# Performance work log

Hardware: AMD Instinct MI355X
Metric: run time of the kernel (lower is better)

## Reference

```python
import jax, jax.numpy as jnp
import numpy as np

WINDOW_SIZE = 11
SIGMA = 1.5
DATA_RANGE = 1.0
CHANNEL = 3
K1 = 0.01
K2 = 0.03
EPS = 1e-08


def _gaussian_window(window_size, sigma, channel):
    # 1D gaussian normalized to sum 1, then outer product -> 2D window
    xs = np.arange(window_size) - window_size // 2
    g = np.exp(-(xs.astype(np.float32) ** 2) / (2.0 * sigma ** 2))
    g = g / g.sum()
    w2d = np.outer(g, g).astype(np.float32)  # [K, K]
    # depthwise kernel in OIHW layout: [channel, 1, K, K]
    return jnp.asarray(np.broadcast_to(w2d, (channel, 1, window_size, window_size)))


def _depthwise_blur(img, window):
    # img: [B, C, H, W], window: [C, 1, K, K]; SAME padding depthwise conv
    pad = WINDOW_SIZE // 2
    return jax.lax.conv_general_dilated(
        img, window,
        window_strides=(1, 1),
        padding=[(pad, pad), (pad, pad)],
        dimension_numbers=("NCHW", "OIHW", "NCHW"),
        feature_group_count=CHANNEL,
    )


def setup_inputs() -> dict:
    key = jax.random.key(0)
    kx, ky = jax.random.split(key)
    x = jax.random.uniform(kx, (32, 3, 512, 512), dtype=jnp.float32)
    y = jax.random.uniform(ky, (32, 3, 512, 512), dtype=jnp.float32)
    return {"x": x, "y": y}


def reference(x, y):
    window = _gaussian_window(WINDOW_SIZE, SIGMA, CHANNEL)
    C1 = (K1 * DATA_RANGE) ** 2
    C2 = (K2 * DATA_RANGE) ** 2

    mu_x = _depthwise_blur(x, window)
    mu_y = _depthwise_blur(y, window)
    mu_x2 = mu_x * mu_x
    mu_y2 = mu_y * mu_y
    mu_xy = mu_x * mu_y

    sigma_x2 = _depthwise_blur(x * x, window) - mu_x2
    sigma_y2 = _depthwise_blur(y * y, window) - mu_y2
    sigma_xy = _depthwise_blur(x * y, window) - mu_xy

    num = (2.0 * mu_xy + C1) * (2.0 * sigma_xy + C2)
    den = (mu_x2 + mu_y2 + C1) * (sigma_x2 + sigma_y2 + C2)
    ssim_map = num / (den + EPS)
    return 1.0 - jnp.mean(ssim_map)
```

## Files before the change

### kernel.cpp

```cpp
#include <hip/hip_runtime.h>

typedef float v4f   __attribute__((ext_vector_type(4)));
typedef float f32x4 __attribute__((ext_vector_type(4)));
typedef _Float16 h4 __attribute__((ext_vector_type(4)));
typedef _Float16 h8 __attribute__((ext_vector_type(8)));

#define HH 512
#define WW 512
#define NPLANES 96
#define NSTRIP 32
#define NUNIT (NPLANES * NSTRIP)
#define WPB 4
#define NBLK (NUNIT / WPB)
#define C1V 1e-4f
#define C2V 9e-4f
#define EPSV 1e-8f
#define NPIX 25165824.0f

#define SLOT_B 640
#define Q_B    1920
#define WAVE_B 9600
#define LDS_B  (WPB * WAVE_B)

#define MF(A, B) __builtin_amdgcn_mfma_f32_16x16x32_f16((A), (B), zf, 0, 0, 0)

#define SELW(DST, IX) { const int ix_ = (IX); float r_ = 0.f; \
  r_ = (ix_ == 0) ? wv0 : r_;  r_ = (ix_ == 1) ? wv1 : r_; \
  r_ = (ix_ == 2) ? wv2 : r_;  r_ = (ix_ == 3) ? wv3 : r_; \
  r_ = (ix_ == 4) ? wv4 : r_;  r_ = (ix_ == 5) ? wv5 : r_; \
  r_ = (ix_ == 6) ? wv6 : r_;  r_ = (ix_ == 7) ? wv7 : r_; \
  r_ = (ix_ == 8) ? wv8 : r_;  r_ = (ix_ == 9) ? wv9 : r_; \
  r_ = (ix_ == 10) ? wv10 : r_; DST = r_; }

#define PACK8(DST, F0,F1,F2,F3,F4,F5,F6,F7) \
  DST = (h8){(_Float16)(F0),(_Float16)(F1),(_Float16)(F2),(_Float16)(F3), \
             (_Float16)(F4),(_Float16)(F5),(_Float16)(F6),(_Float16)(F7)};

#define EPX(M) { \
  const float mux_ = mx[M], muy_ = my[M]; \
  const float mx2_ = mux_ * mux_, my2_ = muy_ * muy_, mxy_ = mux_ * muy_; \
  const float sx2_ = vx2[M] - mx2_, sy2_ = vy2[M] - my2_, sxy_ = vxy[M] - mxy_; \
  const float num_ = fmaf(2.f, mxy_, C1V) * fmaf(2.f, sxy_, C2V); \
  const float den_ = (mx2_ + my2_ + C1V) * (sx2_ + sy2_ + C2V) + EPSV; \
  acc##M = fmaf(num_, __builtin_amdgcn_rcpf(den_), acc##M); }

#define VLOADL(O) { \
  const int c_ = (O) - 1 + ((s + 1) >> 1); \
  const char* rb_ = wlds + ((c_ + 3) % 3) * SLOT_B + rByte; \
  vbx  = *(const h8*)(rb_); \
  vby  = *(const h8*)(rb_ + Q_B); \
  vbx2 = *(const h8*)(rb_ + 2 * Q_B); \
  vby2 = *(const h8*)(rb_ + 3 * Q_B); \
  vbxy = *(const h8*)(rb_ + 4 * Q_B); }

#define VMFMA { \
  const f32x4 mx  = MF(Wf, vbx);  const f32x4 my  = MF(Wf, vby); \
  const f32x4 vx2 = MF(Wf, vbx2); const f32x4 vy2 = MF(Wf, vby2); \
  const f32x4 vxy = MF(Wf, vbxy); \
  EPX(0) EPX(1) EPX(2) EPX(3) }

#define STEP(TT, CXA,CXB,CYA,CYB) { \
  const int tt_ = (TT); \
  if (tt_ >= 3) VLOADL(tt_ - 3) \
  h8 ax, ay; \
  PACK8(ax, CXA[0],CXA[1],CXA[2],CXA[3], CXB[0],CXB[1],CXB[2],CXB[3]) \
  PACK8(ay, CYA[0],CYA[1],CYA[2],CYA[3], CYB[0],CYB[1],CYB[2],CYB[3]) \
  if (tt_ < 32) { \
    const int rb2_ = min(max(16 * (tt_ + 1), 0), 496); \
    const float* qx_ = xp + (size_t)rb2_ * WW; \
    const float* qy_ = yp + (size_t)rb2_ * WW; \
    CXA = *(const v4f*)(qx_ + offA); CXB = *(const v4f*)(qx_ + offB); \
    CYA = *(const v4f*)(qy_ + offA); CYB = *(const v4f*)(qy_ + offB); \
  } \
  const bool rOK_ = (unsigned)(tt_ - 1) < 32u; \
  const h8 wfh_ = rOK_ ? WfH : (h8)(_Float16)0.f; \
  const h8 ax2 = ax * ax, ay2 = ay * ay, axy = ax * ay; \
  const f32x4 chx  = MF(ax,  wfh_); const f32x4 chy  = MF(ay,  wfh_); \
  const f32x4 chx2 = MF(ax2, wfh_); const f32x4 chy2 = MF(ay2, wfh_); \
  const f32x4 chxy = MF(axy, wfh_); \
  { char* wb_ = wlds + ((tt_ + 2) % 3) * SLOT_B + wByte; \
    *(h4*)(wb_)         = (h4){(_Float16)chx[0], (_Float16)chx[1], (_Float16)chx[2], (_Float16)chx[3]}; \
    *(h4*)(wb_ + Q_B)   = (h4){(_Float16)chy[0], (_Float16)chy[1], (_Float16)chy[2], (_Float16)chy[3]}; \
    *(h4*)(wb_ + 2*Q_B) = (h4){(_Float16)chx2[0],(_Float16)chx2[1],(_Float16)chx2[2],(_Float16)chx2[3]}; \
    *(h4*)(wb_ + 3*Q_B) = (h4){(_Float16)chy2[0],(_Float16)chy2[1],(_Float16)chy2[2],(_Float16)chy2[3]}; \
    *(h4*)(wb_ + 4*Q_B) = (h4){(_Float16)chxy[0],(_Float16)chxy[1],(_Float16)chxy[2],(_Float16)chxy[3]}; } \
  if (tt_ >= 3) VMFMA }

__global__ __launch_bounds__(64 * WPB)
void ssim_main(const float* __restrict__ x, const float* __restrict__ y,
               float* __restrict__ partial)
{
  __shared__ __attribute__((aligned(16))) char lds[LDS_B];

  const int l = threadIdx.x & 63;
  const int wid = threadIdx.x >> 6;
  const int n = l & 15;
  const int s = l >> 4;

  const int wg = blockIdx.x;
  const int swz = (wg & 7) * (NBLK / 8) + (wg >> 3);
  const int unit = swz * WPB + wid;
  const int plane = unit >> 5;
  const int strip = unit & 31;
  const int C0 = strip * 16;

  char* wlds = lds + wid * WAVE_B;

  const float* xp = x + (size_t)plane * (HH * WW);
  const float* yp = y + (size_t)plane * (HH * WW);

  float wv0, wv1, wv2, wv3, wv4, wv5, wv6, wv7, wv8, wv9, wv10;
#define WINIT(k) wv##k = expf(-((float)((k - 5) * (k - 5))) / 4.5f);
  WINIT(0) WINIT(1) WINIT(2) WINIT(3) WINIT(4) WINIT(5)
  WINIT(6) WINIT(7) WINIT(8) WINIT(9) WINIT(10)
#undef WINIT
  const float inv_ = 1.f / (wv0 + wv1 + wv2 + wv3 + wv4 + wv5 + wv6 + wv7 + wv8 + wv9 + wv10);
#define WNORM(k) wv##k = __int_as_float(__builtin_amdgcn_readfirstlane(__float_as_int(wv##k * inv_)));
  WNORM(0) WNORM(1) WNORM(2) WNORM(3) WNORM(4) WNORM(5)
  WNORM(6) WNORM(7) WNORM(8) WNORM(9) WNORM(10)
#undef WNORM

  const f32x4 zf = {0.f, 0.f, 0.f, 0.f};

  h8 Wf;
  {
    const int kb = 8 * s;
    float b0,b1,b2,b3,b4,b5,b6,b7;
    SELW(b0, kb + 0 - n - 3) SELW(b1, kb + 1 - n - 3)
    SELW(b2, kb + 2 - n - 3) SELW(b3, kb + 3 - n - 3)
    SELW(b4, kb + 4 - n - 3) SELW(b5, kb + 5 - n - 3)
    SELW(b6, kb + 6 - n - 3) SELW(b7, kb + 7 - n - 3)
    PACK8(Wf, b0,b1,b2,b3,b4,b5,b6,b7)
  }

  const int cb = C0 - 8 + 8 * s;
  const bool kill = (cb < 0) || (cb >= WW);
  h8 WfH = Wf;
  if (kill) WfH = (h8)(_Float16)0.f;
  const int ca = kill ? 0 : cb;

  const int offA = n * WW + ca;
  const int offB = offA + 4;

  const int wByte = n * 40 + 8 * s;
  const int rByte = n * 40 + 16 * ((s + 1) & 1);

  h8 vbx, vby, vbx2, vby2, vbxy;
  float acc0 = 0.f, acc1 = 0.f, acc2 = 0.f, acc3 = 0.f;

  v4f XA0, XB0, YA0, YB0, XA1, XB1, YA1, YB1;
  XA0 = *(const v4f*)(xp + offA); XB0 = *(const v4f*)(xp + offB);
  YA0 = *(const v4f*)(yp + offA); YB0 = *(const v4f*)(yp + offB);
  XA1 = XA0; XB1 = XB0; YA1 = YA0; YB1 = YB0;

  #pragma unroll 1
  for (int u = 0; u < 17; ++u) {
    STEP(2 * u,     XA0, XB0, YA0, YB0)
    STEP(2 * u + 1, XA1, XB1, YA1, YB1)
  }
  VLOADL(31) VMFMA

  float a = (acc0 + acc1) + (acc2 + acc3);
  #pragma unroll
  for (int off = 32; off > 0; off >>= 1) a += __shfl_down(a, off);
  if (l == 0) partial[unit] = a;
}

__global__ void finalize_kernel(const float* __restrict__ partial, float* __restrict__ out)
{
  __shared__ float s4[4];
  float a = 0.f;
  for (int i = threadIdx.x; i < NUNIT; i += 256) a += partial[i];
  #pragma unroll
  for (int off = 32; off > 0; off >>= 1) a += __shfl_down(a, off);
  if ((threadIdx.x & 63) == 0) s4[threadIdx.x >> 6] = a;
  __syncthreads();
  if (threadIdx.x == 0) out[0] = 1.f - (s4[0] + s4[1] + s4[2] + s4[3]) * (1.f / NPIX);
}

extern "C" void kernel_launch(void* const* d_in, const int* in_sizes, int n_in,
                              void* d_out, int out_size, void* d_ws, size_t ws_size,
                              hipStream_t stream)
{
  const float* x = (const float*)d_in[0];
  const float* y = (const float*)d_in[1];
  float* ws = (float*)d_ws;
  float* out = (float*)d_out;

  hipLaunchKernelGGL(ssim_main, dim3(NBLK), dim3(64 * WPB), 0, stream, x, y, ws);
  hipLaunchKernelGGL(finalize_kernel, dim3(1), dim3(256), 0, stream, ws, out);
}
```

Baseline: 74.76 us.

## Split each wave's column strip into two interleaved half-height chains

Each wave now processes its 512-row strip as two independent chains (top and bottom halves) interleaved step by step, each with its own LDS ring and accumulators. Workgroups shrink to two waves and the per-wave LDS doubles, with a waves-per-EU hint added. The goal is more instruction-level parallelism per wave, so MFMA, LDS and global-load latencies of one chain overlap with work from the other. In exchange it raises register pressure, adds halo rows at the chain boundary, and lowers the wave count per block.

```diff
diff --git a/kernel.cpp b/kernel.cpp
--- a/kernel.cpp
+++ b/kernel.cpp
@@ -10,7 +10,7 @@
 #define NPLANES 96
 #define NSTRIP 32
 #define NUNIT (NPLANES * NSTRIP)
-#define WPB 4
+#define WPB 2
 #define NBLK (NUNIT / WPB)
 #define C1V 1e-4f
 #define C2V 9e-4f
@@ -19,7 +19,8 @@
 
 #define SLOT_B 640
 #define Q_B    1920
-#define WAVE_B 9600
+#define CHAIN_B 9600
+#define WAVE_B 19200
 #define LDS_B  (WPB * WAVE_B)
 
 #define MF(A, B) __builtin_amdgcn_mfma_f32_16x16x32_f16((A), (B), zf, 0, 0, 0)
@@ -36,57 +37,63 @@
   DST = (h8){(_Float16)(F0),(_Float16)(F1),(_Float16)(F2),(_Float16)(F3), \
              (_Float16)(F4),(_Float16)(F5),(_Float16)(F6),(_Float16)(F7)};
 
-#define EPX(M) { \
+#define EPX(S, M) { \
   const float mux_ = mx[M], muy_ = my[M]; \
   const float mx2_ = mux_ * mux_, my2_ = muy_ * muy_, mxy_ = mux_ * muy_; \
   const float sx2_ = vx2[M] - mx2_, sy2_ = vy2[M] - my2_, sxy_ = vxy[M] - mxy_; \
   const float num_ = fmaf(2.f, mxy_, C1V) * fmaf(2.f, sxy_, C2V); \
   const float den_ = (mx2_ + my2_ + C1V) * (sx2_ + sy2_ + C2V) + EPSV; \
-  acc##M = fmaf(num_, __builtin_amdgcn_rcpf(den_), acc##M); }
-
-#define VLOADL(O) { \
+  acc##S##M = fmaf(num_, __builtin_amdgcn_rcpf(den_), acc##S##M); }
+
+#define VLOADL(S, O) { \
   const int c_ = (O) - 1 + ((s + 1) >> 1); \
-  const char* rb_ = wlds + ((c_ + 3) % 3) * SLOT_B + rByte; \
-  vbx  = *(const h8*)(rb_); \
-  vby  = *(const h8*)(rb_ + Q_B); \
-  vbx2 = *(const h8*)(rb_ + 2 * Q_B); \
-  vby2 = *(const h8*)(rb_ + 3 * Q_B); \
-  vbxy = *(const h8*)(rb_ + 4 * Q_B); }
-
-#define VMFMA { \
-  const f32x4 mx  = MF(Wf, vbx);  const f32x4 my  = MF(Wf, vby); \
-  const f32x4 vx2 = MF(Wf, vbx2); const f32x4 vy2 = MF(Wf, vby2); \
-  const f32x4 vxy = MF(Wf, vbxy); \
-  EPX(0) EPX(1) EPX(2) EPX(3) }
-
-#define STEP(TT, CXA,CXB,CYA,CYB) { \
+  const char* rb_ = wlds##S + ((c_ + 3) % 3) * SLOT_B + rByte; \
+  vbx##S  = *(const h8*)(rb_); \
+  vby##S  = *(const h8*)(rb_ + Q_B); \
+  vbx2##S = *(const h8*)(rb_ + 2 * Q_B); \
+  vby2##S = *(const h8*)(rb_ + 3 * Q_B); \
+  vbxy##S = *(const h8*)(rb_ + 4 * Q_B); }
+
+#define VMFMA(S) { \
+  const f32x4 mx  = MF(Wf, vbx##S);  const f32x4 my  = MF(Wf, vby##S); \
+  const f32x4 vx2 = MF(Wf, vbx2##S); const f32x4 vy2 = MF(Wf, vby2##S); \
+  const f32x4 vxy = MF(Wf, vbxy##S); \
+  EPX(S, 0) EPX(S, 1) EPX(S, 2) EPX(S, 3) }
+
+#define HSTEP(S, CB, TT, CXA,CXB,CYA,CYB) { \
   const int tt_ = (TT); \
-  if (tt_ >= 3) VLOADL(tt_ - 3) \
   h8 ax, ay; \
   PACK8(ax, CXA[0],CXA[1],CXA[2],CXA[3], CXB[0],CXB[1],CXB[2],CXB[3]) \
   PACK8(ay, CYA[0],CYA[1],CYA[2],CYA[3], CYB[0],CYB[1],CYB[2],CYB[3]) \
-  if (tt_ < 32) { \
-    const int rb2_ = min(max(16 * (tt_ + 1), 0), 496); \
+  if (tt_ < 16) { \
+    const int rb2_ = min(max(16 * (tt_ + 1 + (CB)), 0), 496); \
     const float* qx_ = xp + (size_t)rb2_ * WW; \
     const float* qy_ = yp + (size_t)rb2_ * WW; \
     CXA = *(const v4f*)(qx_ + offA); CXB = *(const v4f*)(qx_ + offB); \
     CYA = *(const v4f*)(qy_ + offA); CYB = *(const v4f*)(qy_ + offB); \
   } \
-  const bool rOK_ = (unsigned)(tt_ - 1) < 32u; \
+  const bool rOK_ = (unsigned)(tt_ - 1 + (CB)) < 32u; \
   const h8 wfh_ = rOK_ ? WfH : (h8)(_Float16)0.f; \
   const h8 ax2 = ax * ax, ay2 = ay * ay, axy = ax * ay; \
   const f32x4 chx  = MF(ax,  wfh_); const f32x4 chy  = MF(ay,  wfh_); \
   const f32x4 chx2 = MF(ax2, wfh_); const f32x4 chy2 = MF(ay2, wfh_); \
   const f32x4 chxy = MF(axy, wfh_); \
-  { char* wb_ = wlds + ((tt_ + 2) % 3) * SLOT_B + wByte; \
+  { char* wb_ = wlds##S + ((tt_ + 2) % 3) * SLOT_B + wByte; \
     *(h4*)(wb_)         = (h4){(_Float16)chx[0], (_Float16)chx[1], (_Float16)chx[2], (_Float16)chx[3]}; \
     *(h4*)(wb_ + Q_B)   = (h4){(_Float16)chy[0], (_Float16)chy[1], (_Float16)chy[2], (_Float16)chy[3]}; \
     *(h4*)(wb_ + 2*Q_B) = (h4){(_Float16)chx2[0],(_Float16)chx2[1],(_Float16)chx2[2],(_Float16)chx2[3]}; \
     *(h4*)(wb_ + 3*Q_B) = (h4){(_Float16)chy2[0],(_Float16)chy2[1],(_Float16)chy2[2],(_Float16)chy2[3]}; \
-    *(h4*)(wb_ + 4*Q_B) = (h4){(_Float16)chxy[0],(_Float16)chxy[1],(_Float16)chxy[2],(_Float16)chxy[3]}; } \
-  if (tt_ >= 3) VMFMA }
+    *(h4*)(wb_ + 4*Q_B) = (h4){(_Float16)chxy[0],(_Float16)chxy[1],(_Float16)chxy[2],(_Float16)chxy[3]}; } }
+
+#define DSTEP(TT, AXA,AXB,AYA,AYB, BXA,BXB,BYA,BYB) { \
+  const int td_ = (TT); \
+  if (td_ >= 3) { VLOADL(A, td_ - 3) VLOADL(B, td_ - 3) } \
+  HSTEP(A, 0,  td_, AXA,AXB,AYA,AYB) \
+  HSTEP(B, 16, td_, BXA,BXB,BYA,BYB) \
+  if (td_ >= 3) { VMFMA(A) VMFMA(B) } }
 
 __global__ __launch_bounds__(64 * WPB)
+__attribute__((amdgpu_waves_per_eu(2)))
 void ssim_main(const float* __restrict__ x, const float* __restrict__ y,
                float* __restrict__ partial)
 {
@@ -104,7 +111,8 @@
   const int strip = unit & 31;
   const int C0 = strip * 16;
 
-  char* wlds = lds + wid * WAVE_B;
+  char* wldsA = lds + wid * WAVE_B;
+  char* wldsB = wldsA + CHAIN_B;
 
   const float* xp = x + (size_t)plane * (HH * WW);
   const float* yp = y + (size_t)plane * (HH * WW);
@@ -145,22 +153,36 @@
   const int wByte = n * 40 + 8 * s;
   const int rByte = n * 40 + 16 * ((s + 1) & 1);
 
-  h8 vbx, vby, vbx2, vby2, vbxy;
-  float acc0 = 0.f, acc1 = 0.f, acc2 = 0.f, acc3 = 0.f;
-
-  v4f XA0, XB0, YA0, YB0, XA1, XB1, YA1, YB1;
-  XA0 = *(const v4f*)(xp + offA); XB0 = *(const v4f*)(xp + offB);
-  YA0 = *(const v4f*)(yp + offA); YB0 = *(const v4f*)(yp + offB);
-  XA1 = XA0; XB1 = XB0; YA1 = YA0; YB1 = YB0;
+  h8 vbxA, vbyA, vbx2A, vby2A, vbxyA, vbxB, vbyB, vbx2B, vby2B, vbxyB;
+  float accA0 = 0.f, accA1 = 0.f, accA2 = 0.f, accA3 = 0.f;
+  float accB0 = 0.f, accB1 = 0.f, accB2 = 0.f, accB3 = 0.f;
+  v4f AXA0, AXB0, AYA0, AYB0, AXA1, AXB1, AYA1, AYB1;
+  v4f BXA0, BXB0, BYA0, BYB0, BXA1, BXB1, BYA1, BYB1;
+
+  AXA0 = *(const v4f*)(xp + offA); AXB0 = *(const v4f*)(xp + offB);
+  AYA0 = *(const v4f*)(yp + offA); AYB0 = *(const v4f*)(yp + offB);
+  AXA1 = AXA0; AXB1 = AXB0; AYA1 = AYA0; AYB1 = AYB0;
+  {
+    const float* q15x = xp + (size_t)240 * WW;
+    const float* q15y = yp + (size_t)240 * WW;
+    const float* q16x = xp + (size_t)256 * WW;
+    const float* q16y = yp + (size_t)256 * WW;
+    BXA0 = *(const v4f*)(q15x + offA); BXB0 = *(const v4f*)(q15x + offB);
+    BYA0 = *(const v4f*)(q15y + offA); BYB0 = *(const v4f*)(q15y + offB);
+    BXA1 = *(const v4f*)(q16x + offA); BXB1 = *(const v4f*)(q16x + offB);
+    BYA1 = *(const v4f*)(q16y + offA); BYB1 = *(const v4f*)(q16y + offB);
+  }
 
   #pragma unroll 1
-  for (int u = 0; u < 17; ++u) {
-    STEP(2 * u,     XA0, XB0, YA0, YB0)
-    STEP(2 * u + 1, XA1, XB1, YA1, YB1)
+  for (int u = 0; u < 9; ++u) {
+    DSTEP(2 * u,     AXA0,AXB0,AYA0,AYB0, BXA0,BXB0,BYA0,BYB0)
+    DSTEP(2 * u + 1, AXA1,AXB1,AYA1,AYB1, BXA1,BXB1,BYA1,BYB1)
   }
-  VLOADL(31) VMFMA
-
-  float a = (acc0 + acc1) + (acc2 + acc3);
+  VLOADL(A, 15) VMFMA(A)
+  VLOADL(B, 15) VMFMA(B)
+
+  float a = ((accA0 + accA1) + (accA2 + accA3))
+          + ((accB0 + accB1) + (accB2 + accB3));
   #pragma unroll
   for (int off = 32; off > 0; off >>= 1) a += __shfl_down(a, off);
   if (l == 0) partial[unit] = a;
```

New measurement: 102.5 us. 1.37x slower.
